# Kernel tuning notes

Hardware: AMD Instinct MI355X
Metric: run time of the kernel (lower is better)

The kernel has to match this reference:

```python
import jax, jax.numpy as jnp
import numpy as np

B, N, D = 4, 4096, 1024
DFF = 4 * D
K = 2048  # max(1, int(N * 0.5))


def setup_inputs() -> dict:
    key = jax.random.key(0)
    ks = jax.random.split(key, 4)
    x = jax.random.normal(ks[0], (B, N, D), dtype=jnp.float32)
    gate_w = jax.random.normal(ks[1], (1, D), dtype=jnp.float32) * 0.02
    w1 = jax.random.normal(ks[2], (D, DFF), dtype=jnp.float32) * (1.0 / np.sqrt(D))
    b1 = jnp.zeros((DFF,), dtype=jnp.float32)
    w2 = jax.random.normal(ks[3], (DFF, D), dtype=jnp.float32) * (1.0 / np.sqrt(DFF))
    b2 = jnp.zeros((D,), dtype=jnp.float32)
    return {"x": x, "gate_w": gate_w, "w1": w1, "b1": b1, "w2": w2, "b2": b2, "k": K}


def reference(x, gate_w, w1, b1, w2, b2, k):
    # scores: [B, N] = gate(x).squeeze(-1)
    scores = jnp.einsum("bnd,d->bn", x, gate_w[0])
    _, topk = jax.lax.top_k(scores, k)          # [B, k] token indices
    # gather selected tokens: [B, k, D]
    x_sel = jnp.take_along_axis(x, topk[:, :, None], axis=1)
    # ffn (d -> 4d -> d, GELU) + residual on selected tokens only
    h = jax.nn.gelu(x_sel @ w1 + b1) @ w2 + b2
    x_proc = x_sel + h
    # scatter processed tokens back into a copy of x
    b_idx = jnp.arange(x.shape[0])[:, None]      # [B, 1]
    out = x.at[b_idx, topk].set(x_proc)
    return out
```

## Files before the change

kernel.cpp:

```cpp
#include <hip/hip_runtime.h>
#include <math.h>

#define B_   4
#define N_   4096
#define D_   1024
#define DFF_ 4096
#define K_   2048

typedef __attribute__((ext_vector_type(8))) short short8;
typedef __attribute__((ext_vector_type(4))) float float4v;

__device__ __forceinline__ unsigned short f2bf(float f) {
    unsigned int u = __float_as_uint(f);
    u = (u + 0x7fffu + ((u >> 16) & 1u)) >> 16;
    return (unsigned short)u;
}

__device__ __forceinline__ void gld16(const void* g, void* l) {
    __builtin_amdgcn_global_load_lds((const __attribute__((address_space(1))) void*)g,
                                     (__attribute__((address_space(3))) void*)l, 16, 0, 0);
}

__global__ __launch_bounds__(256) void scores_transpose_kernel(const float* __restrict__ x,
                                                               const float* __restrict__ gate_w,
                                                               float* __restrict__ scores,
                                                               int* __restrict__ slot,
                                                               const float* __restrict__ w1,
                                                               const float* __restrict__ w2,
                                                               unsigned short* __restrict__ w1t,
                                                               unsigned short* __restrict__ w2t) {
    __shared__ float tile[32][33];
    int bid = blockIdx.x;
    if (bid < 4096) {
        int wave = (bid * 256 + threadIdx.x) >> 6;
        int lane = threadIdx.x & 63;
        if (lane == 1) slot[wave] = -1;
        const float4* xr = (const float4*)(x + (size_t)wave * D_);
        const float4* g  = (const float4*)gate_w;
        float acc = 0.f;
        #pragma unroll
        for (int j = 0; j < D_ / 4 / 64; ++j) {
            float4 a = xr[lane + j * 64];
            float4 b = g[lane + j * 64];
            acc += a.x * b.x + a.y * b.y + a.z * b.z + a.w * b.w;
        }
        #pragma unroll
        for (int off = 32; off > 0; off >>= 1) acc += __shfl_down(acc, off, 64);
        if (lane == 0) scores[wave] = acc;
        return;
    }
    int tb = bid - 4096;
    const float* src; unsigned short* dst; int R, C, bx, by;
    if (tb < 4096) { src = w1; dst = w1t; R = D_;   C = DFF_; bx = tb & 127;          by = tb >> 7; }
    else           { src = w2; dst = w2t; R = DFF_; C = D_;   bx = (tb - 4096) & 31;  by = (tb - 4096) >> 5; }
    int tx = threadIdx.x & 31, ty = threadIdx.x >> 5;
    int c = bx * 32 + tx, r0 = by * 32;
    #pragma unroll
    for (int j = ty; j < 32; j += 8) tile[j][tx] = src[(size_t)(r0 + j) * C + c];
    __syncthreads();
    int dc = by * 32 + tx, dr0 = bx * 32;
    #pragma unroll
    for (int j = ty; j < 32; j += 8) dst[(size_t)(dr0 + j) * R + dc] = f2bf(tile[tx][j]);
}

__global__ __launch_bounds__(1024) void select_topk_kernel(const float* __restrict__ scores,
                                                           int* __restrict__ topk,
                                                           int* __restrict__ slot) {
    __shared__ unsigned key[N_];
    __shared__ unsigned hist[256];
    __shared__ int sh_bin, sh_rem, sh_ngt;
    __shared__ int wsum[16], woff[16];
    int b = blockIdx.x, tid = threadIdx.x;
    int lane = tid & 63, wid = tid >> 6;

    for (int i = tid; i < N_; i += 1024) {
        unsigned u = __float_as_uint(scores[b * N_ + i]);
        key[i] = (u & 0x80000000u) ? ~u : (u | 0x80000000u);
    }
    if (tid == 0) sh_ngt = 0;
    __syncthreads();

    unsigned prefix = 0, pmask = 0;
    int rem = K_;
    for (int shift = 24; shift >= 0; shift -= 8) {
        if (tid < 256) hist[tid] = 0;
        __syncthreads();
        for (int i = tid; i < N_; i += 1024) {
            unsigned k = key[i];
            if ((k & pmask) == prefix) atomicAdd(&hist[(k >> shift) & 255u], 1u);
        }
        __syncthreads();
        if (tid < 64) {
            unsigned v0 = hist[4 * lane], v1 = hist[4 * lane + 1];
            unsigned v2 = hist[4 * lane + 2], v3 = hist[4 * lane + 3];
            unsigned s3 = v3, s2 = v2 + s3, s1 = v1 + s2, s0 = v0 + s1;
            unsigned t = s0;
            #pragma unroll
            for (int off = 1; off < 64; off <<= 1) {
                unsigned u = __shfl_down(t, off, 64);
                if (lane + off < 64) t += u;
            }
            unsigned above = t - s0;
            unsigned S0 = s0 + above, S1 = s1 + above, S2 = s2 + above, S3 = s3 + above;
            unsigned R = (unsigned)rem;
            if (S0 >= R && S1 < R) { sh_bin = 4 * lane;     sh_rem = rem - (int)S1; }
            if (S1 >= R && S2 < R) { sh_bin = 4 * lane + 1; sh_rem = rem - (int)S2; }
            if (S2 >= R && S3 < R) { sh_bin = 4 * lane + 2; sh_rem = rem - (int)S3; }
            if (S3 >= R && above < R) { sh_bin = 4 * lane + 3; sh_rem = rem - (int)above; }
        }
        __syncthreads();
        prefix |= ((unsigned)sh_bin) << shift;
        pmask  |= 0xffu << shift;
        rem = sh_rem;
    }
    unsigned T = prefix;
    int c_gt = K_ - rem;

    for (int i = tid; i < N_; i += 1024) {
        bool p = key[i] > T;
        unsigned long long m = __ballot(p);
        int cnt = __popcll(m);
        int basepos = 0;
        if (lane == 0 && cnt) basepos = atomicAdd(&sh_ngt, cnt);
        basepos = __shfl(basepos, 0, 64);
        if (p) {
            int pos = basepos + __popcll(m & ((1ULL << lane) - 1ULL));
            topk[b * K_ + pos] = i;
            slot[b * N_ + i] = b * K_ + pos;
        }
    }
    int base = tid * 4, c = 0;
    #pragma unroll
    for (int j = 0; j < 4; ++j) c += (key[base + j] == T);
    int sc = c;
    #pragma unroll
    for (int off = 1; off < 64; off <<= 1) {
        int u = __shfl_up(sc, off, 64);
        if (lane >= off) sc += u;
    }
    if (lane == 63) wsum[wid] = sc;
    __syncthreads();
    if (tid == 0) {
        int run = 0;
        #pragma unroll
        for (int j = 0; j < 16; ++j) { woff[j] = run; run += wsum[j]; }
    }
    __syncthreads();
    int r = woff[wid] + sc - c;
    #pragma unroll
    for (int j = 0; j < 4; ++j) {
        if (key[base + j] == T) {
            if (r < rem) {
                topk[b * K_ + c_gt + r] = base + j;
                slot[b * N_ + base + j] = b * K_ + c_gt + r;
            }
            ++r;
        }
    }
}

__global__ __launch_bounds__(256) void gather_copy_kernel(const float* __restrict__ x,
                                                          const int* __restrict__ slot,
                                                          unsigned short* __restrict__ xsel,
                                                          float* __restrict__ out) {
    int row = blockIdx.x;
    int t = threadIdx.x;
    int s = slot[row];
    float4 v = ((const float4*)(x + (size_t)row * D_))[t];
    if (s >= 0) {
        ushort4 o;
        o.x = f2bf(v.x); o.y = f2bf(v.y); o.z = f2bf(v.z); o.w = f2bf(v.w);
        ((ushort4*)(xsel + (size_t)s * D_))[t] = o;
    } else {
        ((float4*)(out + (size_t)row * D_))[t] = v;
    }
}

__global__ __launch_bounds__(256) void ffn1_mfma_kernel(const unsigned short* __restrict__ A,
                                                        const unsigned short* __restrict__ Bt,
                                                        const float* __restrict__ b1,
                                                        unsigned short* __restrict__ h1) {
    constexpr int K = D_;
    __shared__ __align__(16) char smem[16896];
    unsigned short* As = (unsigned short*)smem;
    unsigned short* Bs = As + 4096;
    unsigned short* Cs = (unsigned short*)smem;
    int t = threadIdx.x;
    int w = t >> 6, lane = t & 63;
    int quad = lane >> 4, lr = lane & 15;
    int wm = w >> 1, wn = w & 1;
    int row0 = blockIdx.x * 128, col0 = blockIdx.y * 128;

    const char* ga0 = (const char*)(A + (size_t)(row0 + (t >> 2)) * K) + (t & 3) * 16;
    const char* ga1 = ga0 + (size_t)64 * K * 2;
    const char* gb0 = (const char*)(Bt + (size_t)(col0 + (t >> 2)) * K) + (t & 3) * 16;
    const char* gb1 = gb0 + (size_t)64 * K * 2;
    unsigned short* la0 = As + t * 8;   unsigned short* la1 = As + 2048 + t * 8;
    unsigned short* lb0 = Bs + t * 8;   unsigned short* lb1 = Bs + 2048 + t * 8;

    float4v acc[4][4] = {};
    for (int k0 = 0; k0 < K; k0 += 32) {
        gld16(ga0, la0); gld16(ga1, la1);
        gld16(gb0, lb0); gld16(gb1, lb1);
        ga0 += 64; ga1 += 64; gb0 += 64; gb1 += 64;
        __syncthreads();
        short8 af[4], bfv[4];
        #pragma unroll
        for (int mi = 0; mi < 4; ++mi)
            af[mi] = *(const short8*)(As + (size_t)(wm * 64 + mi * 16 + lr) * 32 + quad * 8);
        #pragma unroll
        for (int ni = 0; ni < 4; ++ni)
            bfv[ni] = *(const short8*)(Bs + (size_t)(wn * 64 + ni * 16 + lr) * 32 + quad * 8);
        #pragma unroll
        for (int mi = 0; mi < 4; ++mi)
            #pragma unroll
            for (int ni = 0; ni < 4; ++ni)
                acc[mi][ni] = __builtin_amdgcn_mfma_f32_16x16x32_bf16(af[mi], bfv[ni], acc[mi][ni], 0, 0, 0);
        __syncthreads();
    }

    #pragma unroll
    for (int half = 0; half < 2; ++half) {
        __syncthreads();
        #pragma unroll
        for (int mi2 = 0; mi2 < 2; ++mi2) {
            int mi = half * 2 + mi2;
            #pragma unroll
            for (int ni = 0; ni < 4; ++ni) {
                int col = wn * 64 + ni * 16 + lr;
                float bias = b1[col0 + col];
                #pragma unroll
                for (int r = 0; r < 4; ++r) {
                    int lrow = wm * 32 + mi2 * 16 + quad * 4 + r;
                    float u = acc[mi][ni][r] + bias;
                    float tt = 1.5957691216057308f * u * (1.0f + 0.044715f * u * u);
                    float g = u / (1.0f + __expf(-tt));
                    Cs[lrow * 132 + col] = f2bf(g);
                }
            }
        }
        __syncthreads();
        #pragma unroll
        for (int kch = 0; kch < 4; ++kch) {
            int ch = t + kch * 256;
            int lrow = ch >> 4;
            int off = (ch & 15) * 8;
            int grow = row0 + ((lrow >> 5) << 6) + half * 32 + (lrow & 31);
            *(short8*)(h1 + (size_t)grow * DFF_ + col0 + off) = *(const short8*)(Cs + lrow * 132 + off);
        }
    }
}

__global__ __launch_bounds__(256) void ffn2_mfma_kernel(const unsigned short* __restrict__ A,
                                                        const unsigned short* __restrict__ Bt,
                                                        const float* __restrict__ b2,
                                                        const float* __restrict__ x,
                                                        const int* __restrict__ topk,
                                                        float* __restrict__ out) {
    constexpr int K = DFF_;
    __shared__ __align__(16) char smem[16896];
    unsigned short* As = (unsigned short*)smem;
    unsigned short* Bs = As + 4096;
    float* Cs = (float*)smem;
    int t = threadIdx.x;
    int w = t >> 6, lane = t & 63;
    int quad = lane >> 4, lr = lane & 15;
    int wm = w >> 1, wn = w & 1;
    int row0 = blockIdx.x * 128, col0 = blockIdx.y * 128;

    const char* ga0 = (const char*)(A + (size_t)(row0 + (t >> 2)) * K) + (t & 3) * 16;
    const char* ga1 = ga0 + (size_t)64 * K * 2;
    const char* gb0 = (const char*)(Bt + (size_t)(col0 + (t >> 2)) * K) + (t & 3) * 16;
    const char* gb1 = gb0 + (size_t)64 * K * 2;
    unsigned short* la0 = As + t * 8;   unsigned short* la1 = As + 2048 + t * 8;
    unsigned short* lb0 = Bs + t * 8;   unsigned short* lb1 = Bs + 2048 + t * 8;

    float4v acc[4][4] = {};
    for (int k0 = 0; k0 < K; k0 += 32) {
        gld16(ga0, la0); gld16(ga1, la1);
        gld16(gb0, lb0); gld16(gb1, lb1);
        ga0 += 64; ga1 += 64; gb0 += 64; gb1 += 64;
        __syncthreads();
        short8 af[4], bfv[4];
        #pragma unroll
        for (int mi = 0; mi < 4; ++mi)
            af[mi] = *(const short8*)(As + (size_t)(wm * 64 + mi * 16 + lr) * 32 + quad * 8);
        #pragma unroll
        for (int ni = 0; ni < 4; ++ni)
            bfv[ni] = *(const short8*)(Bs + (size_t)(wn * 64 + ni * 16 + lr) * 32 + quad * 8);
        #pragma unroll
        for (int mi = 0; mi < 4; ++mi)
            #pragma unroll
            for (int ni = 0; ni < 4; ++ni)
                acc[mi][ni] = __builtin_amdgcn_mfma_f32_16x16x32_bf16(af[mi], bfv[ni], acc[mi][ni], 0, 0, 0);
        __syncthreads();
    }

    #pragma unroll
    for (int q = 0; q < 4; ++q) {
        __syncthreads();
        if (wm == (q >> 1)) {
            #pragma unroll
            for (int mi2 = 0; mi2 < 2; ++mi2) {
                int mi = (q & 1) * 2 + mi2;
                #pragma unroll
                for (int ni = 0; ni < 4; ++ni) {
                    int col = wn * 64 + ni * 16 + lr;
                    #pragma unroll
                    for (int r = 0; r < 4; ++r)
                        Cs[(mi2 * 16 + quad * 4 + r) * 132 + col] = acc[mi][ni][r];
                }
            }
        }
        __syncthreads();
        #pragma unroll
        for (int kch = 0; kch < 4; ++kch) {
            int ch = t + kch * 256;
            int lrow = ch >> 5;
            int c4 = (ch & 31) * 4;
            int grow = row0 + q * 32 + lrow;
            int gb = grow >> 11;
            int tok = topk[grow];
            size_t base = ((size_t)(gb * N_ + tok)) * D_ + col0 + c4;
            float4 xv = *(const float4*)(x + base);
            float4 bv = *(const float4*)(b2 + col0 + c4);
            const float* cp = Cs + lrow * 132 + c4;
            float4 o;
            o.x = xv.x + cp[0] + bv.x;
            o.y = xv.y + cp[1] + bv.y;
            o.z = xv.z + cp[2] + bv.z;
            o.w = xv.w + cp[3] + bv.w;
            *(float4*)(out + base) = o;
        }
    }
}

extern "C" void kernel_launch(void* const* d_in, const int* in_sizes, int n_in,
                              void* d_out, int out_size, void* d_ws, size_t ws_size,
                              hipStream_t stream) {
    const float* x      = (const float*)d_in[0];
    const float* gate_w = (const float*)d_in[1];
    const float* w1     = (const float*)d_in[2];
    const float* b1     = (const float*)d_in[3];
    const float* w2     = (const float*)d_in[4];
    const float* b2     = (const float*)d_in[5];
    float* out = (float*)d_out;

    char* ws = (char*)d_ws;
    float*          scores = (float*)ws;
    int*            topk   = (int*)(ws + (64 << 10));
    int*            slot   = (int*)(ws + (96 << 10));
    unsigned short* xsel   = (unsigned short*)(ws + (160 << 10));
    unsigned short* w1t    = (unsigned short*)(ws + (160 << 10) + (16 << 20));
    unsigned short* w2t    = (unsigned short*)(ws + (160 << 10) + (24 << 20));
    unsigned short* h1     = (unsigned short*)(ws + (160 << 10) + (32 << 20));

    scores_transpose_kernel<<<12288, 256, 0, stream>>>(x, gate_w, scores, slot, w1, w2, w1t, w2t);
    select_topk_kernel<<<B_, 1024, 0, stream>>>(scores, topk, slot);
    gather_copy_kernel<<<B_ * N_, 256, 0, stream>>>(x, slot, xsel, out);

    ffn1_mfma_kernel<<<dim3(64, 32), 256, 0, stream>>>(xsel, w1t, b1, h1);
    ffn2_mfma_kernel<<<dim3(64, 8), 256, 0, stream>>>(h1, w2t, b2, x, topk, out);
}
```

Measured before the change: 358.8 us.

## Split scores/transpose kernels, persistent FFN1 grid, swizzled 64-wide K tiles in FFN2

Separates the gate-score and weight-transpose work into two kernels and launches the transpose after top-k selection. FFN1 becomes a 1024-block grid in which each block loops over two output tiles. FFN2 now stages 64-wide K slices into 32 KB of LDS with an XOR swizzle, meant to halve the barrier count per K step and cut LDS bank conflicts. In exchange FFN2 uses more LDS per block, and the extra kernel launch adds scheduling overhead.

```diff
diff --git a/kernel.cpp b/kernel.cpp
--- a/kernel.cpp
+++ b/kernel.cpp
@@ -21,46 +21,26 @@
                                      (__attribute__((address_space(3))) void*)l, 16, 0, 0);
 }
 
-__global__ __launch_bounds__(256) void scores_transpose_kernel(const float* __restrict__ x,
-                                                               const float* __restrict__ gate_w,
-                                                               float* __restrict__ scores,
-                                                               int* __restrict__ slot,
-                                                               const float* __restrict__ w1,
-                                                               const float* __restrict__ w2,
-                                                               unsigned short* __restrict__ w1t,
-                                                               unsigned short* __restrict__ w2t) {
-    __shared__ float tile[32][33];
-    int bid = blockIdx.x;
-    if (bid < 4096) {
-        int wave = (bid * 256 + threadIdx.x) >> 6;
-        int lane = threadIdx.x & 63;
-        if (lane == 1) slot[wave] = -1;
-        const float4* xr = (const float4*)(x + (size_t)wave * D_);
-        const float4* g  = (const float4*)gate_w;
-        float acc = 0.f;
-        #pragma unroll
-        for (int j = 0; j < D_ / 4 / 64; ++j) {
-            float4 a = xr[lane + j * 64];
-            float4 b = g[lane + j * 64];
-            acc += a.x * b.x + a.y * b.y + a.z * b.z + a.w * b.w;
-        }
-        #pragma unroll
-        for (int off = 32; off > 0; off >>= 1) acc += __shfl_down(acc, off, 64);
-        if (lane == 0) scores[wave] = acc;
-        return;
-    }
-    int tb = bid - 4096;
-    const float* src; unsigned short* dst; int R, C, bx, by;
-    if (tb < 4096) { src = w1; dst = w1t; R = D_;   C = DFF_; bx = tb & 127;          by = tb >> 7; }
-    else           { src = w2; dst = w2t; R = DFF_; C = D_;   bx = (tb - 4096) & 31;  by = (tb - 4096) >> 5; }
-    int tx = threadIdx.x & 31, ty = threadIdx.x >> 5;
-    int c = bx * 32 + tx, r0 = by * 32;
-    #pragma unroll
-    for (int j = ty; j < 32; j += 8) tile[j][tx] = src[(size_t)(r0 + j) * C + c];
-    __syncthreads();
-    int dc = by * 32 + tx, dr0 = bx * 32;
-    #pragma unroll
-    for (int j = ty; j < 32; j += 8) dst[(size_t)(dr0 + j) * R + dc] = f2bf(tile[tx][j]);
+__global__ __launch_bounds__(256) void scores_kernel(const float* __restrict__ x,
+                                                     const float* __restrict__ gate_w,
+                                                     float* __restrict__ scores,
+                                                     int* __restrict__ slot) {
+    int wave = (blockIdx.x * blockDim.x + threadIdx.x) >> 6;
+    int lane = threadIdx.x & 63;
+    if (wave >= B_ * N_) return;
+    if (lane == 1) slot[wave] = -1;
+    const float4* xr = (const float4*)(x + (size_t)wave * D_);
+    const float4* g  = (const float4*)gate_w;
+    float acc = 0.f;
+    #pragma unroll
+    for (int j = 0; j < D_ / 4 / 64; ++j) {
+        float4 a = xr[lane + j * 64];
+        float4 b = g[lane + j * 64];
+        acc += a.x * b.x + a.y * b.y + a.z * b.z + a.w * b.w;
+    }
+    #pragma unroll
+    for (int off = 32; off > 0; off >>= 1) acc += __shfl_down(acc, off, 64);
+    if (lane == 0) scores[wave] = acc;
 }
 
 __global__ __launch_bounds__(1024) void select_topk_kernel(const float* __restrict__ scores,
@@ -157,6 +137,25 @@
             ++r;
         }
     }
+}
+
+__global__ __launch_bounds__(256) void transpose_both_kernel(const float* __restrict__ w1,
+                                                             const float* __restrict__ w2,
+                                                             unsigned short* __restrict__ w1t,
+                                                             unsigned short* __restrict__ w2t) {
+    __shared__ float tile[32][33];
+    int bid = blockIdx.x;
+    const float* src; unsigned short* dst; int R, C, bx, by;
+    if (bid < 4096) { src = w1; dst = w1t; R = D_;   C = DFF_; bx = bid & 127;          by = bid >> 7; }
+    else            { src = w2; dst = w2t; R = DFF_; C = D_;   bx = (bid - 4096) & 31;  by = (bid - 4096) >> 5; }
+    int tx = threadIdx.x & 31, ty = threadIdx.x >> 5;
+    int c = bx * 32 + tx, r0 = by * 32;
+    #pragma unroll
+    for (int j = ty; j < 32; j += 8) tile[j][tx] = src[(size_t)(r0 + j) * C + c];
+    __syncthreads();
+    int dc = by * 32 + tx, dr0 = bx * 32;
+    #pragma unroll
+    for (int j = ty; j < 32; j += 8) dst[(size_t)(dr0 + j) * R + dc] = f2bf(tile[tx][j]);
 }
 
 __global__ __launch_bounds__(256) void gather_copy_kernel(const float* __restrict__ x,
@@ -189,64 +188,69 @@
     int w = t >> 6, lane = t & 63;
     int quad = lane >> 4, lr = lane & 15;
     int wm = w >> 1, wn = w & 1;
-    int row0 = blockIdx.x * 128, col0 = blockIdx.y * 128;
-
-    const char* ga0 = (const char*)(A + (size_t)(row0 + (t >> 2)) * K) + (t & 3) * 16;
-    const char* ga1 = ga0 + (size_t)64 * K * 2;
-    const char* gb0 = (const char*)(Bt + (size_t)(col0 + (t >> 2)) * K) + (t & 3) * 16;
-    const char* gb1 = gb0 + (size_t)64 * K * 2;
     unsigned short* la0 = As + t * 8;   unsigned short* la1 = As + 2048 + t * 8;
     unsigned short* lb0 = Bs + t * 8;   unsigned short* lb1 = Bs + 2048 + t * 8;
 
-    float4v acc[4][4] = {};
-    for (int k0 = 0; k0 < K; k0 += 32) {
-        gld16(ga0, la0); gld16(ga1, la1);
-        gld16(gb0, lb0); gld16(gb1, lb1);
-        ga0 += 64; ga1 += 64; gb0 += 64; gb1 += 64;
-        __syncthreads();
-        short8 af[4], bfv[4];
-        #pragma unroll
-        for (int mi = 0; mi < 4; ++mi)
-            af[mi] = *(const short8*)(As + (size_t)(wm * 64 + mi * 16 + lr) * 32 + quad * 8);
-        #pragma unroll
-        for (int ni = 0; ni < 4; ++ni)
-            bfv[ni] = *(const short8*)(Bs + (size_t)(wn * 64 + ni * 16 + lr) * 32 + quad * 8);
-        #pragma unroll
-        for (int mi = 0; mi < 4; ++mi)
+    for (int tile = blockIdx.x; tile < 2048; tile += 1024) {
+        int row0 = (tile & 63) * 128;
+        int col0 = (tile >> 6) * 128;
+        __syncthreads();
+
+        const char* ga0 = (const char*)(A + (size_t)(row0 + (t >> 2)) * K) + (t & 3) * 16;
+        const char* ga1 = ga0 + (size_t)64 * K * 2;
+        const char* gb0 = (const char*)(Bt + (size_t)(col0 + (t >> 2)) * K) + (t & 3) * 16;
+        const char* gb1 = gb0 + (size_t)64 * K * 2;
+
+        float4v acc[4][4] = {};
+        for (int k0 = 0; k0 < K; k0 += 32) {
+            gld16(ga0, la0); gld16(ga1, la1);
+            gld16(gb0, lb0); gld16(gb1, lb1);
+            ga0 += 64; ga1 += 64; gb0 += 64; gb1 += 64;
+            __syncthreads();
+            short8 af[4], bfv[4];
+            #pragma unroll
+            for (int mi = 0; mi < 4; ++mi)
+                af[mi] = *(const short8*)(As + (size_t)(wm * 64 + mi * 16 + lr) * 32 + quad * 8);
             #pragma unroll
             for (int ni = 0; ni < 4; ++ni)
-                acc[mi][ni] = __builtin_amdgcn_mfma_f32_16x16x32_bf16(af[mi], bfv[ni], acc[mi][ni], 0, 0, 0);
-        __syncthreads();
-    }
-
-    #pragma unroll
-    for (int half = 0; half < 2; ++half) {
-        __syncthreads();
-        #pragma unroll
-        for (int mi2 = 0; mi2 < 2; ++mi2) {
-            int mi = half * 2 + mi2;
-            #pragma unroll
-            for (int ni = 0; ni < 4; ++ni) {
-                int col = wn * 64 + ni * 16 + lr;
-                float bias = b1[col0 + col];
+                bfv[ni] = *(const short8*)(Bs + (size_t)(wn * 64 + ni * 16 + lr) * 32 + quad * 8);
+            #pragma unroll
+            for (int mi = 0; mi < 4; ++mi)
                 #pragma unroll
-                for (int r = 0; r < 4; ++r) {
-                    int lrow = wm * 32 + mi2 * 16 + quad * 4 + r;
-                    float u = acc[mi][ni][r] + bias;
-                    float tt = 1.5957691216057308f * u * (1.0f + 0.044715f * u * u);
-                    float g = u / (1.0f + __expf(-tt));
-                    Cs[lrow * 132 + col] = f2bf(g);
+                for (int ni = 0; ni < 4; ++ni)
+                    acc[mi][ni] = __builtin_amdgcn_mfma_f32_16x16x32_bf16(af[mi], bfv[ni], acc[mi][ni], 0, 0, 0);
+            __syncthreads();
+        }
+
+        #pragma unroll
+        for (int half = 0; half < 2; ++half) {
+            __syncthreads();
+            #pragma unroll
+            for (int mi2 = 0; mi2 < 2; ++mi2) {
+                int mi = half * 2 + mi2;
+                #pragma unroll
+                for (int ni = 0; ni < 4; ++ni) {
+                    int col = wn * 64 + ni * 16 + lr;
+                    float bias = b1[col0 + col];
+                    #pragma unroll
+                    for (int r = 0; r < 4; ++r) {
+                        int lrow = wm * 32 + mi2 * 16 + quad * 4 + r;
+                        float u = acc[mi][ni][r] + bias;
+                        float tt = 1.5957691216057308f * u * (1.0f + 0.044715f * u * u);
+                        float g = u / (1.0f + __expf(-tt));
+                        Cs[lrow * 132 + col] = f2bf(g);
+                    }
                 }
             }
-        }
-        __syncthreads();
-        #pragma unroll
-        for (int kch = 0; kch < 4; ++kch) {
-            int ch = t + kch * 256;
-            int lrow = ch >> 4;
-            int off = (ch & 15) * 8;
-            int grow = row0 + ((lrow >> 5) << 6) + half * 32 + (lrow & 31);
-            *(short8*)(h1 + (size_t)grow * DFF_ + col0 + off) = *(const short8*)(Cs + lrow * 132 + off);
+            __syncthreads();
+            #pragma unroll
+            for (int kch = 0; kch < 4; ++kch) {
+                int ch = t + kch * 256;
+                int lrow = ch >> 4;
+                int off = (ch & 15) * 8;
+                int grow = row0 + ((lrow >> 5) << 6) + half * 32 + (lrow & 31);
+                *(short8*)(h1 + (size_t)grow * DFF_ + col0 + off) = *(const short8*)(Cs + lrow * 132 + off);
+            }
         }
     }
 }
@@ -258,9 +262,9 @@
                                                         const int* __restrict__ topk,
                                                         float* __restrict__ out) {
     constexpr int K = DFF_;
-    __shared__ __align__(16) char smem[16896];
+    __shared__ __align__(16) char smem[32768];
     unsigned short* As = (unsigned short*)smem;
-    unsigned short* Bs = As + 4096;
+    unsigned short* Bs = As + 8192;
     float* Cs = (float*)smem;
     int t = threadIdx.x;
     int w = t >> 6, lane = t & 63;
@@ -268,31 +272,47 @@
     int wm = w >> 1, wn = w & 1;
     int row0 = blockIdx.x * 128, col0 = blockIdx.y * 128;
 
-    const char* ga0 = (const char*)(A + (size_t)(row0 + (t >> 2)) * K) + (t & 3) * 16;
-    const char* ga1 = ga0 + (size_t)64 * K * 2;
-    const char* gb0 = (const char*)(Bt + (size_t)(col0 + (t >> 2)) * K) + (t & 3) * 16;
-    const char* gb1 = gb0 + (size_t)64 * K * 2;
-    unsigned short* la0 = As + t * 8;   unsigned short* la1 = As + 2048 + t * 8;
-    unsigned short* lb0 = Bs + t * 8;   unsigned short* lb1 = Bs + 2048 + t * 8;
+    const unsigned short* ga[4]; const unsigned short* gb[4];
+    unsigned short* la[4]; unsigned short* lb[4];
+    #pragma unroll
+    for (int jj = 0; jj < 4; ++jj) {
+        int ci = jj * 256 + t;
+        int rr = ci >> 3;
+        int kcs = (ci & 7) ^ (rr & 7);
+        ga[jj] = A  + (size_t)(row0 + rr) * K + kcs * 8;
+        gb[jj] = Bt + (size_t)(col0 + rr) * K + kcs * 8;
+        la[jj] = As + ci * 8;
+        lb[jj] = Bs + ci * 8;
+    }
 
     float4v acc[4][4] = {};
-    for (int k0 = 0; k0 < K; k0 += 32) {
-        gld16(ga0, la0); gld16(ga1, la1);
-        gld16(gb0, lb0); gld16(gb1, lb1);
-        ga0 += 64; ga1 += 64; gb0 += 64; gb1 += 64;
-        __syncthreads();
-        short8 af[4], bfv[4];
-        #pragma unroll
-        for (int mi = 0; mi < 4; ++mi)
-            af[mi] = *(const short8*)(As + (size_t)(wm * 64 + mi * 16 + lr) * 32 + quad * 8);
-        #pragma unroll
-        for (int ni = 0; ni < 4; ++ni)
-            bfv[ni] = *(const short8*)(Bs + (size_t)(wn * 64 + ni * 16 + lr) * 32 + quad * 8);
-        #pragma unroll
-        for (int mi = 0; mi < 4; ++mi)
-            #pragma unroll
-            for (int ni = 0; ni < 4; ++ni)
-                acc[mi][ni] = __builtin_amdgcn_mfma_f32_16x16x32_bf16(af[mi], bfv[ni], acc[mi][ni], 0, 0, 0);
+    for (int k0 = 0; k0 < K; k0 += 64) {
+        #pragma unroll
+        for (int jj = 0; jj < 4; ++jj) {
+            gld16(ga[jj], la[jj]); gld16(gb[jj], lb[jj]);
+            ga[jj] += 64; gb[jj] += 64;
+        }
+        __syncthreads();
+        #pragma unroll
+        for (int kk = 0; kk < 2; ++kk) {
+            int c = kk * 4 + quad;
+            short8 af[4], bfv[4];
+            #pragma unroll
+            for (int mi = 0; mi < 4; ++mi) {
+                int r = wm * 64 + mi * 16 + lr;
+                af[mi] = *(const short8*)(As + ((size_t)r * 8 + (c ^ (r & 7))) * 8);
+            }
+            #pragma unroll
+            for (int ni = 0; ni < 4; ++ni) {
+                int r = wn * 64 + ni * 16 + lr;
+                bfv[ni] = *(const short8*)(Bs + ((size_t)r * 8 + (c ^ (r & 7))) * 8);
+            }
+            #pragma unroll
+            for (int mi = 0; mi < 4; ++mi)
+                #pragma unroll
+                for (int ni = 0; ni < 4; ++ni)
+                    acc[mi][ni] = __builtin_amdgcn_mfma_f32_16x16x32_bf16(af[mi], bfv[ni], acc[mi][ni], 0, 0, 0);
+        }
         __syncthreads();
     }
 
@@ -319,9 +339,9 @@
             int lrow = ch >> 5;
             int c4 = (ch & 31) * 4;
             int grow = row0 + q * 32 + lrow;
-            int gb = grow >> 11;
+            int gb2 = grow >> 11;
             int tok = topk[grow];
-            size_t base = ((size_t)(gb * N_ + tok)) * D_ + col0 + c4;
+            size_t base = ((size_t)(gb2 * N_ + tok)) * D_ + col0 + c4;
             float4 xv = *(const float4*)(x + base);
             float4 bv = *(const float4*)(b2 + col0 + c4);
             const float* cp = Cs + lrow * 132 + c4;
@@ -355,10 +375,11 @@
     unsigned short* w2t    = (unsigned short*)(ws + (160 << 10) + (24 << 20));
     unsigned short* h1     = (unsigned short*)(ws + (160 << 10) + (32 << 20));
 
-    scores_transpose_kernel<<<12288, 256, 0, stream>>>(x, gate_w, scores, slot, w1, w2, w1t, w2t);
+    scores_kernel<<<(B_ * N_) / 4, 256, 0, stream>>>(x, gate_w, scores, slot);
     select_topk_kernel<<<B_, 1024, 0, stream>>>(scores, topk, slot);
+    transpose_both_kernel<<<8192, 256, 0, stream>>>(w1, w2, w1t, w2t);
     gather_copy_kernel<<<B_ * N_, 256, 0, stream>>>(x, slot, xsel, out);
 
-    ffn1_mfma_kernel<<<dim3(64, 32), 256, 0, stream>>>(xsel, w1t, b1, h1);
+    ffn1_mfma_kernel<<<1024, 256, 0, stream>>>(xsel, w1t, b1, h1);
     ffn2_mfma_kernel<<<dim3(64, 8), 256, 0, stream>>>(h1, w2t, b2, x, topk, out);
 }
```

New measurement: 364.7 us. About the same (+1.7%).
